# Optimization experiments

Measured on AMD Instinct MI355X. Metric: run time of the kernel, lower is better.

## Reference

```python
import jax, jax.numpy as jnp
import numpy as np

N_V = 6890  # SMPL vertices
N_J = 24    # SMPL joints
# standard SMPL kinematic tree: PARENT[i-1] is parent of joint i (i=1..23)
PARENT = np.array([0, 0, 0, 1, 2, 3, 4, 5, 6, 7, 8, 9, 9, 9, 12, 13, 14, 16, 17, 18, 19, 20, 21], dtype=np.int64)


def rodrigues(r):
    """Axis-angle [N,3] -> rotation matrices [N,3,3] (batch Rodrigues)."""
    angle = jnp.sqrt(jnp.sum(r * r, axis=-1, keepdims=True) + 1e-8)  # [N,1]
    axis = r / angle
    c = jnp.cos(angle)[..., None]  # [N,1,1]
    s = jnp.sin(angle)[..., None]
    x, y, z = axis[..., 0], axis[..., 1], axis[..., 2]
    zeros = jnp.zeros_like(x)
    K = jnp.stack([zeros, -z, y, z, zeros, -x, -y, x, zeros], axis=-1).reshape(-1, 3, 3)
    outer = axis[..., :, None] * axis[..., None, :]
    I = jnp.eye(3, dtype=r.dtype)
    return c * I + (1.0 - c) * outer + s * K


def setup_inputs() -> dict:
    key = jax.random.key(0)
    ks = jax.random.split(key, 7)
    B = 1024
    pose = jax.random.normal(ks[0], (B, 72), dtype=jnp.float32) * 0.4
    beta = jax.random.normal(ks[1], (B, 10), dtype=jnp.float32)
    shapedirs = jax.random.normal(ks[2], (N_V, 3, 10), dtype=jnp.float32) * 0.03
    posedirs = jax.random.normal(ks[3], (N_V, 3, 207), dtype=jnp.float32) * 0.01
    v_template = jax.random.normal(ks[4], (N_V, 3), dtype=jnp.float32)
    Jreg = jax.random.uniform(ks[5], (N_J, N_V), dtype=jnp.float32)
    J_regressor = Jreg / jnp.sum(Jreg, axis=1, keepdims=True)  # rows sum to 1 like SMPL
    w = jax.random.uniform(ks[6], (N_V, N_J), dtype=jnp.float32)
    weights = w / jnp.sum(w, axis=1, keepdims=True)  # convex skinning weights
    return {"pose": pose, "beta": beta, "shapedirs": shapedirs, "posedirs": posedirs,
            "v_template": v_template, "J_regressor": J_regressor, "weights": weights}


def reference(pose, beta, shapedirs, posedirs, v_template, J_regressor, weights):
    B = pose.shape[0]
    # shape blend shapes: v_shaped = shapedirs @ beta + template  [B,6890,3]
    v_shaped = jnp.einsum('vcs,bs->bvc', shapedirs, beta) + v_template[None]
    J = jnp.einsum('jv,bvc->bjc', J_regressor, v_shaped)
    # pose -> rotation matrices
    R = rodrigues(pose.reshape(-1, 3)).reshape(B, N_J, 3, 3)
    # pose blend shapes from (R - I) of non-root joints  [B,207]
    lrotmin = (R[:, 1:] - jnp.eye(3, dtype=R.dtype)).reshape(B, 207)
    v_posed = v_shaped + jnp.einsum('vcp,bp->bvc', posedirs, lrotmin)
    # relative joint locations
    J_rel = jnp.concatenate([J[:, :1], J[:, 1:] - J[:, PARENT]], axis=1)  # [B,24,3]
    # local transforms [B,24,4,4]
    G_top = jnp.concatenate([R, J_rel[..., None]], axis=-1)  # [B,24,3,4]
    pad_row = jnp.broadcast_to(jnp.array([0., 0., 0., 1.], dtype=R.dtype), (B, N_J, 1, 4))
    G_local = jnp.concatenate([G_top, pad_row], axis=2)
    # forward kinematics along the chain (fixed 24-joint loop)
    Gs = [G_local[:, 0]]
    for i in range(1, N_J):
        Gs.append(jnp.matmul(Gs[PARENT[i - 1]], G_local[:, i]))
    G = jnp.stack(Gs, axis=1)  # [B,24,4,4]
    # remove rest-pose transform: subtract G @ [J,0] from last column
    J_h = jnp.concatenate([J, jnp.zeros((B, N_J, 1), dtype=J.dtype)], axis=2)  # [B,24,4]
    corr = jnp.einsum('bjmn,bjn->bjm', G, J_h)  # [B,24,4]
    G = G - jnp.pad(corr[..., None], ((0, 0), (0, 0), (0, 0), (3, 0)))
    # skinning: per-vertex transform T = weights @ G  [B,6890,4,4]
    T = jnp.einsum('vj,bjmn->bvmn', weights, G)
    v_h = jnp.concatenate([v_posed, jnp.ones((B, N_V, 1), dtype=v_posed.dtype)], axis=-1)
    v = jnp.einsum('bvmn,bvn->bvm', T, v_h)[..., :3]
    return v
```

## Files before the change

kernel.cpp:

```cpp
#include <hip/hip_runtime.h>
#include <hip/hip_bf16.h>

#define N_V 6890
#define NVPAD 6912
#define N_J 24
#define NREAL 20670
#define NPROWS 27648
#define KDIM 224
#define FB 64
#define FV 32
#define SHP 132
#define NXT 216
#define XCHUNK 27

typedef __attribute__((ext_vector_type(8))) short bf16x8;
typedef __attribute__((ext_vector_type(4))) float f32x4;

__constant__ int c_par[23] = {0,0,0,1,2,3,4,5,6,7,8,9,9,9,12,13,14,16,17,18,19,20,21};

static __device__ __forceinline__ unsigned short f2bf(float f) {
    unsigned int u = __float_as_uint(f);
    unsigned int r = (u + 0x7fffu + ((u >> 16) & 1u)) >> 16;
    return (unsigned short)r;
}
static __device__ __forceinline__ unsigned int pkbf(float a, float b) {
    return ((__float_as_uint(a) + 0x8000u) >> 16) |
           ((__float_as_uint(b) + 0x8000u) & 0xffff0000u);
}
static __device__ __forceinline__ size_t fragidx(int r, int k) {
    return ((size_t)((r >> 4) * 7 + (k >> 5)) << 9) +
           ((size_t)((r & 15) + (((k >> 3) & 3) << 4)) << 3) + (k & 7);
}

#define WS_PARTIAL 0
#define WS_USHORT  7128
#define U_AMF  0
#define U_BPF  229376
#define U_GBF  6422528
#define U_WBF  6946816

#define JREG_BLOCKS 192
#define BPF_BLOCKS  (NPROWS / 16)
#define WBF_BLOCKS  (NVPAD * 32 / 256)

static __device__ __forceinline__ float bval(const float* pd, const float* sd,
                                             const float* vt, int nc, int k) {
    if (k < 207)  return pd[(size_t)nc * 207 + k];
    if (k < 217)  return sd[(size_t)nc * 10 + (k - 207)];
    if (k == 217) return vt[nc];
    return 0.f;
}

__global__ __launch_bounds__(256)
void k_pre(const float* __restrict__ Jreg,
           const float* __restrict__ shapedirs,
           const float* __restrict__ v_template,
           const float* __restrict__ posedirs,
           const float* __restrict__ weights,
           float* __restrict__ partial,
           unsigned short* __restrict__ Bpf,
           unsigned short* __restrict__ Wbf) {
    const int bid = blockIdx.x;
    const int tid = threadIdx.x;

    if (bid < JREG_BLOCKS) {
        const int j = bid >> 3, chunk = bid & 7;
        const int per = (N_V + 7) / 8;
        const int v0 = chunk * per;
        const int v1 = (v0 + per < N_V) ? (v0 + per) : N_V;
        float acc[33];
#pragma unroll
        for (int k = 0; k < 33; ++k) acc[k] = 0.f;
        for (int v = v0 + tid; v < v1; v += 256) {
            const float w = Jreg[j * N_V + v];
            const float* sd = shapedirs + (size_t)v * 30;
#pragma unroll
            for (int k = 0; k < 30; ++k) acc[k] += w * sd[k];
            acc[30] += w * v_template[v * 3 + 0];
            acc[31] += w * v_template[v * 3 + 1];
            acc[32] += w * v_template[v * 3 + 2];
        }
#pragma unroll
        for (int k = 0; k < 33; ++k) {
            float x = acc[k];
            for (int off = 32; off > 0; off >>= 1) x += __shfl_down(x, off);
            acc[k] = x;
        }
        __shared__ float red[4][33];
        const int wave = tid >> 6, lane = tid & 63;
        if (lane == 0) {
#pragma unroll
            for (int k = 0; k < 33; ++k) red[wave][k] = acc[k];
        }
        __syncthreads();
        if (tid < 33) {
            partial[(j * 8 + chunk) * 33 + tid] =
                red[0][tid] + red[1][tid] + red[2][tid] + red[3][tid];
        }
    } else if (bid < JREG_BLOCKS + BPF_BLOCKS) {
        __shared__ float tile[16][228];
        const int r16 = bid - JREG_BLOCKS;
        for (int idx = tid; idx < 16 * 224; idx += 256) {
            const int row = idx / 224;
            const int k = idx - row * 224;
            const int np = r16 * 16 + row;
            const int v = np >> 2, cc = np & 3;
            float val = 0.f;
            if (cc < 3 && v < N_V) val = bval(posedirs, shapedirs, v_template, v * 3 + cc, k);
            tile[row][k] = val;
        }
        __syncthreads();
        const int l = tid >> 2;
        const int row = l & 15;
        const int kblk = (l >> 4) * 8;
        const int e2 = (tid & 3) * 2;
        unsigned short* dst = Bpf + ((size_t)r16 * 7) * 512 + (size_t)tid * 2;
#pragma unroll
        for (int ks = 0; ks < 7; ++ks) {
            const int k = ks * 32 + kblk + e2;
            ushort2 o;
            o.x = f2bf(tile[row][k]);
            o.y = f2bf(tile[row][k + 1]);
            *(ushort2*)(dst + (size_t)ks * 512) = o;
        }
    } else {
        const int idx = (bid - JREG_BLOCKS - BPF_BLOCKS) * 256 + tid;
        const int v = idx >> 5, k = idx & 31;
        float val = (v < N_V && k < 24) ? weights[(size_t)v * 24 + k] : 0.f;
        Wbf[idx] = f2bf(val);
    }
}

__global__ __launch_bounds__(64)
void k_joints(const float* __restrict__ pose, const float* __restrict__ beta,
              const float* __restrict__ partial,
              unsigned short* __restrict__ Amf,
              unsigned short* __restrict__ Gbf) {
    const int b = blockIdx.x;
    const int j = threadIdx.x;
    __shared__ float sJS[24][30];
    __shared__ float sJt[24][3];
    __shared__ float sJ[24][3];
    __shared__ float sG[24][12];

    for (int idx = j; idx < 792; idx += 64) {
        const int jj = idx / 33, kk = idx - jj * 33;
        float s = 0.f;
#pragma unroll
        for (int c = 0; c < 8; ++c) s += partial[(jj * 8 + c) * 33 + kk];
        if (kk < 30) sJS[jj][kk] = s;
        else         sJt[jj][kk - 30] = s;
    }

    for (int idx = j; idx < 224; idx += 64) {
        int mn, jj;
        if (idx < 128) { mn = 12 + (idx >> 5); jj = idx & 31; }
        else { const int q = idx - 128; mn = q >> 3; jj = 24 + (q & 7); }
        Gbf[(size_t)b * 512 + mn * 32 + jj] = 0;
    }
    __syncthreads();

    float R[9];
    if (j < 24) {
        const float* bt = beta + b * 10;
#pragma unroll
        for (int c = 0; c < 3; ++c) {
            float s = sJt[j][c];
#pragma unroll
            for (int t = 0; t < 10; ++t) s += sJS[j][c * 10 + t] * bt[t];
            sJ[j][c] = s;
        }
        const float rx = pose[b * 72 + 3 * j + 0];
        const float ry = pose[b * 72 + 3 * j + 1];
        const float rz = pose[b * 72 + 3 * j + 2];
        const float ang = sqrtf(rx * rx + ry * ry + rz * rz + 1e-8f);
        const float inv = 1.f / ang;
        const float x = rx * inv, y = ry * inv, z = rz * inv;
        const float c = cosf(ang), s = sinf(ang);
        const float ic = 1.f - c;
        R[0] = c + ic * x * x;     R[1] = ic * x * y - s * z; R[2] = ic * x * z + s * y;
        R[3] = ic * x * y + s * z; R[4] = c + ic * y * y;     R[5] = ic * y * z - s * x;
        R[6] = ic * x * z - s * y; R[7] = ic * y * z + s * x; R[8] = c + ic * z * z;
        if (j >= 1) {
            const int kb = (j - 1) * 9;
#pragma unroll
            for (int k = 0; k < 9; ++k)
                Amf[fragidx(b & 15, kb + k) + (size_t)(b >> 4) * 3584] =
                    f2bf(R[k] - ((k == 0 || k == 4 || k == 8) ? 1.f : 0.f));
        }
    } else if (j < 41) {
        const int k = 207 + (j - 24);
        float val = (k < 217) ? beta[b * 10 + (k - 207)] : (k == 217 ? 1.f : 0.f);
        Amf[fragidx(b & 15, k) + (size_t)(b >> 4) * 3584] = f2bf(val);
    }
    __syncthreads();
    if (j < 24) {
        float t0, t1, t2;
        if (j == 0) { t0 = sJ[0][0]; t1 = sJ[0][1]; t2 = sJ[0][2]; }
        else {
            const int p = c_par[j - 1];
            t0 = sJ[j][0] - sJ[p][0]; t1 = sJ[j][1] - sJ[p][1]; t2 = sJ[j][2] - sJ[p][2];
        }
        sG[j][0] = R[0]; sG[j][1] = R[1]; sG[j][2]  = R[2]; sG[j][3]  = t0;
        sG[j][4] = R[3]; sG[j][5] = R[4]; sG[j][6]  = R[5]; sG[j][7]  = t1;
        sG[j][8] = R[6]; sG[j][9] = R[7]; sG[j][10] = R[8]; sG[j][11] = t2;
    }
    __syncthreads();
    if (j == 0) {
        for (int i = 1; i < 24; ++i) {
            const int p = c_par[i - 1];
            float P[12], L[12];
#pragma unroll
            for (int k = 0; k < 12; ++k) { P[k] = sG[p][k]; L[k] = sG[i][k]; }
#pragma unroll
            for (int m = 0; m < 3; ++m) {
#pragma unroll
                for (int n = 0; n < 3; ++n)
                    sG[i][m * 4 + n] = P[m * 4] * L[n] + P[m * 4 + 1] * L[4 + n] + P[m * 4 + 2] * L[8 + n];
                sG[i][m * 4 + 3] = P[m * 4] * L[3] + P[m * 4 + 1] * L[7] + P[m * 4 + 2] * L[11] + P[m * 4 + 3];
            }
        }
    }
    __syncthreads();
    if (j < 24) {
        const float jx = sJ[j][0], jy = sJ[j][1], jz = sJ[j][2];
#pragma unroll
        for (int m = 0; m < 3; ++m) {
            const float corr = sG[j][m * 4] * jx + sG[j][m * 4 + 1] * jy + sG[j][m * 4 + 2] * jz;
            Gbf[(size_t)b * 512 + (m * 4 + 0) * 32 + j] = f2bf(sG[j][m * 4 + 0]);
            Gbf[(size_t)b * 512 + (m * 4 + 1) * 32 + j] = f2bf(sG[j][m * 4 + 1]);
            Gbf[(size_t)b * 512 + (m * 4 + 2) * 32 + j] = f2bf(sG[j][m * 4 + 2]);
            Gbf[(size_t)b * 512 + (m * 4 + 3) * 32 + j] = f2bf(sG[j][m * 4 + 3] - corr);
        }
    }
}

__global__ __launch_bounds__(256, 4)
void k_fused(const unsigned short* __restrict__ Amf,
             const unsigned short* __restrict__ Bpf,
             const unsigned short* __restrict__ Gbf,
             const unsigned short* __restrict__ Wbf,
             float* __restrict__ out) {
    __shared__ unsigned short sH[FB * SHP];
    const int tid = threadIdx.x;
    const int wid = tid >> 6, l = tid & 63;
    const int c16 = l & 15, p = l >> 4;
    const int vh = wid >> 1;
    const int wc = (wid & 1) * 32;

    const int d = blockIdx.x;
    const int q = d >> 3;
    const int xt = (d & 7) * XCHUNK + (q % XCHUNK);
    const int yb = q / XCHUNK;
    const int v0 = xt * FV;
    const int b0 = yb * FB;

    const bf16x8 bw0 = *(const bf16x8*)&Wbf[(size_t)(v0 + c16) * 32 + p * 8];
    const bf16x8 bw1 = *(const bf16x8*)&Wbf[(size_t)(v0 + 16 + c16) * 32 + p * 8];
    const int bwv = wid * 16;
    const unsigned short* gG = Gbf + (size_t)(b0 + bwv) * 512 + c16 * 32 + p * 8;

    f32x4 acc[4][2];
#pragma unroll
    for (int i = 0; i < 4; ++i)
#pragma unroll
        for (int j = 0; j < 2; ++j) acc[i][j] = (f32x4){0.f, 0.f, 0.f, 0.f};

    const unsigned short* pbf = Bpf + ((size_t)(xt * 8 + vh * 4) * 7) * 512 + (size_t)l * 8;
    const unsigned short* pam = Amf + ((size_t)((b0 >> 4) + (wid & 1) * 2) * 7) * 512 + (size_t)l * 8;

#pragma unroll
    for (int ks = 0; ks < 7; ++ks) {
        bf16x8 af[4], bfr[2];
#pragma unroll
        for (int mi = 0; mi < 4; ++mi)
            af[mi] = *(const bf16x8*)(pbf + (size_t)(mi * 7 + ks) * 512);
#pragma unroll
        for (int bj = 0; bj < 2; ++bj)
            bfr[bj] = *(const bf16x8*)(pam + (size_t)(bj * 7 + ks) * 512);
#pragma unroll
        for (int mi = 0; mi < 4; ++mi)
#pragma unroll
            for (int bj = 0; bj < 2; ++bj)
                acc[mi][bj] = __builtin_amdgcn_mfma_f32_16x16x32_bf16(af[mi], bfr[bj], acc[mi][bj], 0, 0, 0);
    }

    bf16x8 agA[8], agB[8];
#pragma unroll
    for (int j = 0; j < 8; ++j)
        agA[j] = *(const bf16x8*)(gG + (size_t)j * 512);

    {
        const int vbase = vh * 16 + p;
#pragma unroll
        for (int mi = 0; mi < 4; ++mi) {
#pragma unroll
            for (int bj = 0; bj < 2; ++bj) {
                const int vl = vbase + mi * 4;
                const int bl = wc + bj * 16 + c16;
                uint2 u;
                u.x = pkbf(acc[mi][bj][0], acc[mi][bj][1]);
                u.y = pkbf(acc[mi][bj][2], acc[mi][bj][3]);
                *(uint2*)&sH[bl * SHP + vl * 4] = u;
            }
        }
    }
    __syncthreads();

#pragma unroll
    for (int j = 0; j < 8; ++j)
        agB[j] = *(const bf16x8*)(gG + (size_t)(8 + j) * 512);

    const bool st0 = (v0 + c16 < N_V) && (p < 3);
    const bool st1 = (v0 + 16 + c16 < N_V) && (p < 3);
    const unsigned short* sh = &sH[bwv * SHP + c16 * 4];
    float* o0 = out + (size_t)(b0 + bwv) * NREAL + (size_t)(v0 + c16) * 3 + p;
    float* o1 = o0 + 48;

#pragma unroll
    for (int j = 0; j < 8; ++j) {
        const f32x4 t0 = __builtin_amdgcn_mfma_f32_16x16x32_bf16(agA[j], bw0, (f32x4){0.f,0.f,0.f,0.f}, 0, 0, 0);
        const f32x4 t1 = __builtin_amdgcn_mfma_f32_16x16x32_bf16(agA[j], bw1, (f32x4){0.f,0.f,0.f,0.f}, 0, 0, 0);
        const uint2 h0 = *(const uint2*)(sh + j * SHP);
        const uint2 h1 = *(const uint2*)(sh + j * SHP + 64);
        const float x0 = __uint_as_float(h0.x << 16);
        const float y0 = __uint_as_float(h0.x & 0xffff0000u);
        const float z0 = __uint_as_float(h0.y << 16);
        const float x1 = __uint_as_float(h1.x << 16);
        const float y1 = __uint_as_float(h1.x & 0xffff0000u);
        const float z1 = __uint_as_float(h1.y << 16);
        const float r0 = t0[0] * x0 + t0[1] * y0 + t0[2] * z0 + t0[3];
        const float r1 = t1[0] * x1 + t1[1] * y1 + t1[2] * z1 + t1[3];
        if (st0) o0[(size_t)j * NREAL] = r0;
        if (st1) o1[(size_t)j * NREAL] = r1;
    }
#pragma unroll
    for (int j = 0; j < 8; ++j) {
        const f32x4 t0 = __builtin_amdgcn_mfma_f32_16x16x32_bf16(agB[j], bw0, (f32x4){0.f,0.f,0.f,0.f}, 0, 0, 0);
        const f32x4 t1 = __builtin_amdgcn_mfma_f32_16x16x32_bf16(agB[j], bw1, (f32x4){0.f,0.f,0.f,0.f}, 0, 0, 0);
        const uint2 h0 = *(const uint2*)(sh + (8 + j) * SHP);
        const uint2 h1 = *(const uint2*)(sh + (8 + j) * SHP + 64);
        const float x0 = __uint_as_float(h0.x << 16);
        const float y0 = __uint_as_float(h0.x & 0xffff0000u);
        const float z0 = __uint_as_float(h0.y << 16);
        const float x1 = __uint_as_float(h1.x << 16);
        const float y1 = __uint_as_float(h1.x & 0xffff0000u);
        const float z1 = __uint_as_float(h1.y << 16);
        const float r0 = t0[0] * x0 + t0[1] * y0 + t0[2] * z0 + t0[3];
        const float r1 = t1[0] * x1 + t1[1] * y1 + t1[2] * z1 + t1[3];
        if (st0) o0[(size_t)(8 + j) * NREAL] = r0;
        if (st1) o1[(size_t)(8 + j) * NREAL] = r1;
    }
}

extern "C" void kernel_launch(void* const* d_in, const int* in_sizes, int n_in,
                              void* d_out, int out_size, void* d_ws, size_t ws_size,
                              hipStream_t stream) {
    const float* pose       = (const float*)d_in[0];
    const float* beta       = (const float*)d_in[1];
    const float* shapedirs  = (const float*)d_in[2];
    const float* posedirs   = (const float*)d_in[3];
    const float* v_template = (const float*)d_in[4];
    const float* Jreg       = (const float*)d_in[5];
    const float* weights    = (const float*)d_in[6];
    float* out = (float*)d_out;

    const int B = in_sizes[0] / 72;

    float* ws = (float*)d_ws;
    float* partial = ws + WS_PARTIAL;
    unsigned short* ubase = (unsigned short*)(ws + WS_USHORT);
    unsigned short* Amf = ubase + U_AMF;
    unsigned short* Bpf = ubase + U_BPF;
    unsigned short* Gbf = ubase + U_GBF;
    unsigned short* Wbf = ubase + U_WBF;

    k_pre<<<JREG_BLOCKS + BPF_BLOCKS + WBF_BLOCKS, 256, 0, stream>>>(
        Jreg, shapedirs, v_template, posedirs, weights, partial, Bpf, Wbf);
    k_joints<<<B, 64, 0, stream>>>(pose, beta, partial, Amf, Gbf);
    k_fused<<<NXT * (B / FB), 256, 0, stream>>>(Amf, Bpf, Gbf, Wbf, out);
}
```

Before: 82.50 us.

## Widen fused kernel vertex tile to 64 and remap block-to-tile scheduling

Doubles the per-block vertex tile from 32 to 64 so each wave computes a 64x64 pose-blend GEMM tile (4x4 MFMA accumulators) and skins four vertex groups per batch row instead of two. The block index is now remapped as an XCD-striped 108x16 grid instead of the chunked 216-tile mapping. This halves the block count and cuts redundant loads of the per-batch A fragments and G matrices, at the cost of more registers and LDS per block, which may lower occupancy.

```diff
diff --git a/kernel.cpp b/kernel.cpp
--- a/kernel.cpp
+++ b/kernel.cpp
@@ -8,10 +8,9 @@
 #define NPROWS 27648
 #define KDIM 224
 #define FB 64
-#define FV 32
-#define SHP 132
-#define NXT 216
-#define XCHUNK 27
+#define FV 64
+#define SHP 260
+#define NXT 108
 
 typedef __attribute__((ext_vector_type(8))) short bf16x8;
 typedef __attribute__((ext_vector_type(4))) float f32x4;
@@ -245,43 +244,42 @@
     const int tid = threadIdx.x;
     const int wid = tid >> 6, l = tid & 63;
     const int c16 = l & 15, p = l >> 4;
-    const int vh = wid >> 1;
-    const int wc = (wid & 1) * 32;
-
-    const int d = blockIdx.x;
-    const int q = d >> 3;
-    const int xt = (d & 7) * XCHUNK + (q % XCHUNK);
-    const int yb = q / XCHUNK;
+
+    const int wg = ((blockIdx.x & 7) * 216) + (blockIdx.x >> 3);
+    const int xt = wg >> 4;
+    const int bg = wg & 15;
     const int v0 = xt * FV;
-    const int b0 = yb * FB;
-
-    const bf16x8 bw0 = *(const bf16x8*)&Wbf[(size_t)(v0 + c16) * 32 + p * 8];
-    const bf16x8 bw1 = *(const bf16x8*)&Wbf[(size_t)(v0 + 16 + c16) * 32 + p * 8];
+    const int b0 = bg * FB;
+
+    bf16x8 bw[4];
+#pragma unroll
+    for (int g = 0; g < 4; ++g)
+        bw[g] = *(const bf16x8*)&Wbf[(size_t)(v0 + g * 16 + c16) * 32 + p * 8];
     const int bwv = wid * 16;
     const unsigned short* gG = Gbf + (size_t)(b0 + bwv) * 512 + c16 * 32 + p * 8;
 
-    f32x4 acc[4][2];
+    f32x4 acc[4][4];
 #pragma unroll
     for (int i = 0; i < 4; ++i)
 #pragma unroll
-        for (int j = 0; j < 2; ++j) acc[i][j] = (f32x4){0.f, 0.f, 0.f, 0.f};
-
-    const unsigned short* pbf = Bpf + ((size_t)(xt * 8 + vh * 4) * 7) * 512 + (size_t)l * 8;
-    const unsigned short* pam = Amf + ((size_t)((b0 >> 4) + (wid & 1) * 2) * 7) * 512 + (size_t)l * 8;
+        for (int j = 0; j < 4; ++j) acc[i][j] = (f32x4){0.f, 0.f, 0.f, 0.f};
+
+    const unsigned short* pbf = Bpf + ((size_t)(xt * 16 + wid * 4) * 7) * 512 + (size_t)l * 8;
+    const unsigned short* pam = Amf + ((size_t)(bg * 4) * 7) * 512 + (size_t)l * 8;
 
 #pragma unroll
     for (int ks = 0; ks < 7; ++ks) {
-        bf16x8 af[4], bfr[2];
+        bf16x8 af[4], bfr[4];
 #pragma unroll
         for (int mi = 0; mi < 4; ++mi)
             af[mi] = *(const bf16x8*)(pbf + (size_t)(mi * 7 + ks) * 512);
 #pragma unroll
-        for (int bj = 0; bj < 2; ++bj)
+        for (int bj = 0; bj < 4; ++bj)
             bfr[bj] = *(const bf16x8*)(pam + (size_t)(bj * 7 + ks) * 512);
 #pragma unroll
         for (int mi = 0; mi < 4; ++mi)
 #pragma unroll
-            for (int bj = 0; bj < 2; ++bj)
+            for (int bj = 0; bj < 4; ++bj)
                 acc[mi][bj] = __builtin_amdgcn_mfma_f32_16x16x32_bf16(af[mi], bfr[bj], acc[mi][bj], 0, 0, 0);
     }
 
@@ -291,13 +289,13 @@
         agA[j] = *(const bf16x8*)(gG + (size_t)j * 512);
 
     {
-        const int vbase = vh * 16 + p;
+        const int vbase = wid * 16 + p;
 #pragma unroll
         for (int mi = 0; mi < 4; ++mi) {
 #pragma unroll
-            for (int bj = 0; bj < 2; ++bj) {
+            for (int bj = 0; bj < 4; ++bj) {
                 const int vl = vbase + mi * 4;
-                const int bl = wc + bj * 16 + c16;
+                const int bl = bj * 16 + c16;
                 uint2 u;
                 u.x = pkbf(acc[mi][bj][0], acc[mi][bj][1]);
                 u.y = pkbf(acc[mi][bj][2], acc[mi][bj][3]);
@@ -311,45 +309,40 @@
     for (int j = 0; j < 8; ++j)
         agB[j] = *(const bf16x8*)(gG + (size_t)(8 + j) * 512);
 
-    const bool st0 = (v0 + c16 < N_V) && (p < 3);
-    const bool st1 = (v0 + 16 + c16 < N_V) && (p < 3);
+    bool st[4];
+    float* o[4];
+#pragma unroll
+    for (int g = 0; g < 4; ++g) {
+        st[g] = (v0 + g * 16 + c16 < N_V) && (p < 3);
+        o[g] = out + (size_t)(b0 + bwv) * NREAL + (size_t)(v0 + g * 16 + c16) * 3 + p;
+    }
     const unsigned short* sh = &sH[bwv * SHP + c16 * 4];
-    float* o0 = out + (size_t)(b0 + bwv) * NREAL + (size_t)(v0 + c16) * 3 + p;
-    float* o1 = o0 + 48;
 
 #pragma unroll
     for (int j = 0; j < 8; ++j) {
-        const f32x4 t0 = __builtin_amdgcn_mfma_f32_16x16x32_bf16(agA[j], bw0, (f32x4){0.f,0.f,0.f,0.f}, 0, 0, 0);
-        const f32x4 t1 = __builtin_amdgcn_mfma_f32_16x16x32_bf16(agA[j], bw1, (f32x4){0.f,0.f,0.f,0.f}, 0, 0, 0);
-        const uint2 h0 = *(const uint2*)(sh + j * SHP);
-        const uint2 h1 = *(const uint2*)(sh + j * SHP + 64);
-        const float x0 = __uint_as_float(h0.x << 16);
-        const float y0 = __uint_as_float(h0.x & 0xffff0000u);
-        const float z0 = __uint_as_float(h0.y << 16);
-        const float x1 = __uint_as_float(h1.x << 16);
-        const float y1 = __uint_as_float(h1.x & 0xffff0000u);
-        const float z1 = __uint_as_float(h1.y << 16);
-        const float r0 = t0[0] * x0 + t0[1] * y0 + t0[2] * z0 + t0[3];
-        const float r1 = t1[0] * x1 + t1[1] * y1 + t1[2] * z1 + t1[3];
-        if (st0) o0[(size_t)j * NREAL] = r0;
-        if (st1) o1[(size_t)j * NREAL] = r1;
+#pragma unroll
+        for (int g = 0; g < 4; ++g) {
+            const f32x4 t = __builtin_amdgcn_mfma_f32_16x16x32_bf16(agA[j], bw[g], (f32x4){0.f,0.f,0.f,0.f}, 0, 0, 0);
+            const uint2 h = *(const uint2*)(sh + j * SHP + g * 64);
+            const float x = __uint_as_float(h.x << 16);
+            const float y = __uint_as_float(h.x & 0xffff0000u);
+            const float z = __uint_as_float(h.y << 16);
+            const float r = t[0] * x + t[1] * y + t[2] * z + t[3];
+            if (st[g]) o[g][(size_t)j * NREAL] = r;
+        }
     }
 #pragma unroll
     for (int j = 0; j < 8; ++j) {
-        const f32x4 t0 = __builtin_amdgcn_mfma_f32_16x16x32_bf16(agB[j], bw0, (f32x4){0.f,0.f,0.f,0.f}, 0, 0, 0);
-        const f32x4 t1 = __builtin_amdgcn_mfma_f32_16x16x32_bf16(agB[j], bw1, (f32x4){0.f,0.f,0.f,0.f}, 0, 0, 0);
-        const uint2 h0 = *(const uint2*)(sh + (8 + j) * SHP);
-        const uint2 h1 = *(const uint2*)(sh + (8 + j) * SHP + 64);
-        const float x0 = __uint_as_float(h0.x << 16);
-        const float y0 = __uint_as_float(h0.x & 0xffff0000u);
-        const float z0 = __uint_as_float(h0.y << 16);
-        const float x1 = __uint_as_float(h1.x << 16);
-        const float y1 = __uint_as_float(h1.x & 0xffff0000u);
-        const float z1 = __uint_as_float(h1.y << 16);
-        const float r0 = t0[0] * x0 + t0[1] * y0 + t0[2] * z0 + t0[3];
-        const float r1 = t1[0] * x1 + t1[1] * y1 + t1[2] * z1 + t1[3];
-        if (st0) o0[(size_t)(8 + j) * NREAL] = r0;
-        if (st1) o1[(size_t)(8 + j) * NREAL] = r1;
+#pragma unroll
+        for (int g = 0; g < 4; ++g) {
+            const f32x4 t = __builtin_amdgcn_mfma_f32_16x16x32_bf16(agB[j], bw[g], (f32x4){0.f,0.f,0.f,0.f}, 0, 0, 0);
+            const uint2 h = *(const uint2*)(sh + (8 + j) * SHP + g * 64);
+            const float x = __uint_as_float(h.x << 16);
+            const float y = __uint_as_float(h.x & 0xffff0000u);
+            const float z = __uint_as_float(h.y << 16);
+            const float r = t[0] * x + t[1] * y + t[2] * z + t[3];
+            if (st[g]) o[g][(size_t)(8 + j) * NREAL] = r;
+        }
     }
 }
 
```

New measurement: 87.62 us. 6.2% more time.
